# Kernel tuning notes

Hardware: AMD Instinct MI355X
Metric: run time of the kernel (lower is better)

## Reference

```python
import jax, jax.numpy as jnp
import numpy as np

N_NODES = 2176
N_IN = 64
N_HID = 2048
N_OUT = 64
NODE_DIM = 64
HEADS = 4


def _build_edge_index():
    hs, os_ = N_IN, N_IN + N_HID
    # input -> hidden block (order: for i: for h)
    s1 = np.repeat(np.arange(0, N_IN), N_HID)
    t1 = np.tile(np.arange(hs, os_), N_IN)
    # hidden -> output block (order: for h: for o)
    s2 = np.repeat(np.arange(hs, os_), N_OUT)
    t2 = np.tile(np.arange(os_, N_NODES), N_HID)
    return jnp.asarray(np.stack([np.concatenate([s1, s2]), np.concatenate([t1, t2])]), dtype=jnp.int32)


def setup_inputs() -> dict:
    key = jax.random.key(0)
    ks = jax.random.split(key, 20)
    D, H = NODE_DIM, HEADS
    edge_index = _build_edge_index()  # [2, E]
    E = edge_index.shape[1]

    def xavier(k, shape):
        fan_in, fan_out = shape[0], shape[1]
        lim = float(np.sqrt(6.0 / (fan_in + fan_out)))
        return jax.random.uniform(k, shape, jnp.float32, -lim, lim)

    return {
        "x_input": jax.random.normal(ks[0], (N_IN,), jnp.float32),
        "node_features": jax.random.normal(ks[1], (N_NODES, D), jnp.float32) * 0.1,
        "edge_weights": jax.random.normal(ks[2], (E, 1), jnp.float32) * 0.1,
        "edge_index": edge_index,
        "wq1": xavier(ks[3], (D, D * H)), "wk1": xavier(ks[4], (D, D * H)),
        "wv1": xavier(ks[5], (D, D * H)), "we1": xavier(ks[6], (1, H)),
        "wo1": xavier(ks[7], (D * H, D)), "bo1": jnp.zeros((D,), jnp.float32),
        "wq2": xavier(ks[8], (D, D * H)), "wk2": xavier(ks[9], (D, D * H)),
        "wv2": xavier(ks[10], (D, D * H)), "we2": xavier(ks[11], (1, H)),
        "wo2": xavier(ks[12], (D * H, D)), "bo2": jnp.zeros((D,), jnp.float32),
        "wproj": xavier(ks[13], (D, 1)), "bproj": jnp.zeros((1,), jnp.float32),
        "num_output_nodes": N_OUT,
    }


def _message_pass(x, edge_index, ew, wq, wk, wv, we, wo, bo):
    # x: [N, D_in]; edge_index: [2, E]; ew: [E, 1]
    src, tgt = edge_index[0], edge_index[1]
    dout = wo.shape[1]
    heads = wq.shape[1] // dout
    q = (x[tgt] @ wq).reshape(-1, heads, dout)  # [E, H, D]
    k = (x[src] @ wk).reshape(-1, heads, dout)
    v = (x[src] @ wv).reshape(-1, heads, dout)
    attn = (q * k).sum(-1) / jnp.sqrt(jnp.float32(dout)) + ew @ we  # [E, H]
    # NOTE: the per-target segment-softmax in the torch source is dead code;
    # the effective math is leaky_relu then a global softmax over edges.
    attn = jax.nn.leaky_relu(attn, negative_slope=0.2)
    attn = jax.nn.softmax(attn, axis=0)
    weighted_v = (attn[:, :, None] * v).reshape(-1, heads * dout)  # [E, H*D]
    out = jax.ops.segment_sum(weighted_v, tgt, num_segments=x.shape[0])  # [N, H*D]
    out = out @ wo + bo
    return out + x  # residual (in_channels == out_channels)


def reference(x_input, node_features, edge_weights, edge_index,
              wq1, wk1, wv1, we1, wo1, bo1,
              wq2, wk2, wv2, we2, wo2, bo2,
              wproj, bproj, num_output_nodes):
    n_in = x_input.shape[0]
    x = node_features.at[:n_in, 0].set(x_input)
    x = jax.nn.relu(_message_pass(x, edge_index, edge_weights, wq1, wk1, wv1, we1, wo1, bo1))
    x = jax.nn.relu(_message_pass(x, edge_index, edge_weights, wq2, wk2, wv2, we2, wo2, bo2))
    out_nodes = x[x.shape[0] - num_output_nodes:]
    output = jax.nn.sigmoid(out_nodes @ wproj + bproj).squeeze()
    return output, x
```

## Files before the change

kernel.cpp:

```cpp
#include <hip/hip_runtime.h>
#include <math.h>

#define E1 131072

__device__ __forceinline__ void gemm_nn_acc(const float* __restrict__ A,
                                            const float* __restrict__ B,
                                            float acc[4][4], int tr, int tc) {
  for (int k4 = 0; k4 < 16; ++k4) {
    float4 b0 = *(const float4*)&B[(k4 * 4 + 0) * 68 + tc * 4];
    float4 b1 = *(const float4*)&B[(k4 * 4 + 1) * 68 + tc * 4];
    float4 b2 = *(const float4*)&B[(k4 * 4 + 2) * 68 + tc * 4];
    float4 b3 = *(const float4*)&B[(k4 * 4 + 3) * 68 + tc * 4];
#pragma unroll
    for (int a = 0; a < 4; ++a) {
      float4 av = *(const float4*)&A[(tr + 16 * a) * 68 + k4 * 4];
      acc[a][0] += av.x * b0.x + av.y * b1.x + av.z * b2.x + av.w * b3.x;
      acc[a][1] += av.x * b0.y + av.y * b1.y + av.z * b2.y + av.w * b3.y;
      acc[a][2] += av.x * b0.z + av.y * b1.z + av.z * b2.z + av.w * b3.z;
      acc[a][3] += av.x * b0.w + av.y * b1.w + av.z * b2.w + av.w * b3.w;
    }
  }
}

__device__ __forceinline__ void gemm_nt_acc(const float* __restrict__ A,
                                            const float* __restrict__ B,
                                            float acc[4][4], int tr, int tc) {
  for (int k4 = 0; k4 < 16; ++k4) {
    float4 av[4], bv[4];
#pragma unroll
    for (int a = 0; a < 4; ++a) av[a] = *(const float4*)&A[(tr + 16 * a) * 68 + k4 * 4];
#pragma unroll
    for (int b = 0; b < 4; ++b) bv[b] = *(const float4*)&B[(tc + 16 * b) * 68 + k4 * 4];
#pragma unroll
    for (int a = 0; a < 4; ++a)
#pragma unroll
      for (int b = 0; b < 4; ++b)
        acc[a][b] += av[a].x * bv[b].x + av[a].y * bv[b].y +
                     av[a].z * bv[b].z + av[a].w * bv[b].w;
  }
}

__device__ __forceinline__ void st_tile(float* __restrict__ C, const float acc[4][4],
                                        int tr, int tc) {
#pragma unroll
  for (int a = 0; a < 4; ++a)
    *(float4*)&C[(tr + 16 * a) * 68 + tc * 4] =
        make_float4(acc[a][0], acc[a][1], acc[a][2], acc[a][3]);
}

__device__ __forceinline__ void ld_x(float* __restrict__ dst, const float* __restrict__ src,
                                     int tid, bool sub, const float* __restrict__ xinp) {
  for (int t4 = tid; t4 < 1024; t4 += 256) {
    int r = t4 >> 4, c0 = (t4 & 15) * 4;
    float4 v = *(const float4*)(src + t4 * 4);
    if (sub && c0 == 0) v.x = xinp[r];
    *(float4*)&dst[r * 68 + c0] = v;
  }
}

__device__ __forceinline__ void ld_w(float* __restrict__ dst, const float* __restrict__ w,
                                     int h, int tid) {
  for (int t4 = tid; t4 < 1024; t4 += 256) {
    int k = t4 >> 4, c0 = (t4 & 15) * 4;
    *(float4*)&dst[k * 68 + c0] = *(const float4*)(w + k * 256 + h * 64 + c0);
  }
}

__global__ __launch_bounds__(256) void k_attn1(const float* __restrict__ x,
                                               const float* __restrict__ xinp,
                                               const float* __restrict__ wq1,
                                               const float* __restrict__ wk1,
                                               const float* __restrict__ we1,
                                               const float* __restrict__ ew,
                                               const float* __restrict__ wq2,
                                               const float* __restrict__ wk2,
                                               const float* __restrict__ wv1,
                                               const float* __restrict__ wo1,
                                               const float* __restrict__ wv2,
                                               const float* __restrict__ wo2,
                                               float* __restrict__ AggH,
                                               float* __restrict__ part,
                                               float* __restrict__ bsum,
                                               float* __restrict__ Mb,
                                               float* __restrict__ W2b) {
  __shared__ float A[4352];
  __shared__ float B[4352];
  __shared__ float C[4352];
  __shared__ float D[4352];
  __shared__ float Ew[4352];
  __shared__ float F[4352];
  __shared__ float G[4352];
  __shared__ float wred[4];
  const int bid = blockIdx.x, tid = threadIdx.x;
  const bool r1 = bid < 128;
  const int tile = (r1 ? bid : bid - 128) >> 2;
  const int h = bid & 3;
  const int j0 = tile * 64;
  const int rowSrc = r1 ? 0 : (64 + j0);
  const int rowQ = r1 ? (64 + j0) : 2112;
  const int tr = tid >> 4, tc = tid & 15;
  const float weh = we1[h];

  ld_x(A, x + rowSrc * 64, tid, r1, xinp);
  ld_x(B, x + rowQ * 64, tid, false, nullptr);
  ld_w(Ew, wk1, h, tid);
  ld_w(F, wq1, h, tid);
  if (r1) {
    for (int t4 = tid; t4 < 1024; t4 += 256) {
      int i = t4 >> 4, jl0 = (t4 & 15) * 4;
      *(float4*)&G[i * 68 + jl0] = *(const float4*)(ew + i * 2048 + j0 + jl0);
    }
  } else {
    for (int t4 = tid; t4 < 1024; t4 += 256) {
      int jl = t4 >> 4, o0 = (t4 & 15) * 4;
      *(float4*)&G[jl * 68 + o0] = *(const float4*)(ew + E1 + (j0 + jl) * 64 + o0);
    }
  }
  __syncthreads();

  {
    float kt[4][4];
#pragma unroll
    for (int a = 0; a < 4; ++a)
#pragma unroll
      for (int q = 0; q < 4; ++q) kt[a][q] = 0.f;
    gemm_nn_acc(A, Ew, kt, tr, tc);
    st_tile(C, kt, tr, tc);
    float qt[4][4];
#pragma unroll
    for (int a = 0; a < 4; ++a)
#pragma unroll
      for (int q = 0; q < 4; ++q) qt[a][q] = 0.f;
    gemm_nn_acc(B, F, qt, tr, tc);
    st_tile(D, qt, tr, tc);
  }
  __syncthreads();

  float acc[4][4];
#pragma unroll
  for (int a = 0; a < 4; ++a)
#pragma unroll
    for (int b = 0; b < 4; ++b) acc[a][b] = 0.f;
  gemm_nt_acc(D, C, acc, tr, tc);
  float esum = 0.f;
#pragma unroll
  for (int a = 0; a < 4; ++a) {
    int row = tr + 16 * a;
#pragma unroll
    for (int b = 0; b < 4; ++b) {
      int col = tc + 16 * b;
      float v = acc[a][b] * 0.125f + G[col * 68 + row] * weh;
      v = (v >= 0.f) ? v : 0.2f * v;
      v = fminf(v, 60.f);
      float e = __expf(v);
      esum += e;
      B[row * 68 + col] = e;
    }
  }
#pragma unroll
  for (int s = 1; s < 64; s <<= 1) esum += __shfl_xor(esum, s);
  if ((tid & 63) == 0) wred[tid >> 6] = esum;
  __syncthreads();

  float u[4][4];
#pragma unroll
  for (int a = 0; a < 4; ++a)
#pragma unroll
    for (int q = 0; q < 4; ++q) u[a][q] = 0.f;
  gemm_nn_acc(B, A, u, tr, tc);
  if (r1) {
#pragma unroll
    for (int a = 0; a < 4; ++a)
      *(float4*)&AggH[(j0 + tr + 16 * a) * 256 + h * 64 + tc * 4] =
          make_float4(u[a][0], u[a][1], u[a][2], u[a][3]);
  } else {
#pragma unroll
    for (int a = 0; a < 4; ++a)
      *(float4*)&part[tile * 16384 + (tr + 16 * a) * 256 + h * 64 + tc * 4] =
          make_float4(u[a][0], u[a][1], u[a][2], u[a][3]);
  }
  if (tid == 0) bsum[bid] = (wred[0] + wred[1]) + (wred[2] + wred[3]);

  if (bid < 12) {
    __syncthreads();
    const int type = bid >> 2, hh = bid & 3;
    if (type == 0) {
      for (int t4 = tid; t4 < 1024; t4 += 256) {
        int r = t4 >> 4, c0 = (t4 & 15) * 4;
        *(float4*)&A[r * 68 + c0] = *(const float4*)(wq2 + r * 256 + hh * 64 + c0);
        *(float4*)&B[r * 68 + c0] = *(const float4*)(wk2 + r * 256 + hh * 64 + c0);
      }
      __syncthreads();
      float m[4][4];
#pragma unroll
      for (int a = 0; a < 4; ++a)
#pragma unroll
        for (int b = 0; b < 4; ++b) m[a][b] = 0.f;
      gemm_nt_acc(A, B, m, tr, tc);
#pragma unroll
      for (int a = 0; a < 4; ++a)
#pragma unroll
        for (int b = 0; b < 4; ++b)
          Mb[hh * 4096 + (tr + 16 * a) * 64 + tc + 16 * b] = m[a][b];
    } else {
      const float* wv = (type == 1) ? wv1 : wv2;
      const float* wo = (type == 1) ? wo1 : wo2;
      for (int t4 = tid; t4 < 1024; t4 += 256) {
        int r = t4 >> 4, c0 = (t4 & 15) * 4;
        *(float4*)&A[r * 68 + c0] = *(const float4*)(wv + r * 256 + hh * 64 + c0);
        *(float4*)&B[r * 68 + c0] = *(const float4*)(wo + (hh * 64 + r) * 64 + c0);
      }
      __syncthreads();
      float m[4][4];
#pragma unroll
      for (int a = 0; a < 4; ++a)
#pragma unroll
        for (int b = 0; b < 4; ++b) m[a][b] = 0.f;
      gemm_nn_acc(A, B, m, tr, tc);
      float* o = W2b + (type - 1) * 16384;
#pragma unroll
      for (int a = 0; a < 4; ++a)
        *(float4*)&o[(hh * 64 + tr + 16 * a) * 64 + tc * 4] =
            make_float4(m[a][0], m[a][1], m[a][2], m[a][3]);
    }
  }
}

__global__ __launch_bounds__(256) void k_attn2(const float* __restrict__ x,
                                               const float* __restrict__ Mb,
                                               const float* __restrict__ we,
                                               const float* __restrict__ ew,
                                               float* __restrict__ AggH,
                                               float* __restrict__ part,
                                               float* __restrict__ bsum) {
  __shared__ float A[4352];
  __shared__ float B[4352];
  __shared__ float C[4352];
  __shared__ float D[4352];
  __shared__ float Em[4352];
  __shared__ float wred[4];
  const int bid = blockIdx.x, tid = threadIdx.x;
  const bool r1 = bid < 128;
  const int tile = (r1 ? bid : bid - 128) >> 2;
  const int h = bid & 3;
  const int j0 = tile * 64;
  const int rowSrc = r1 ? 0 : (64 + j0);
  const int rowQ = r1 ? (64 + j0) : 2112;
  const int tr = tid >> 4, tc = tid & 15;
  const float weh = we[h];
  const float* Mh = Mb + h * 4096;

  ld_x(A, x + rowSrc * 64, tid, false, nullptr);
  ld_x(B, x + rowQ * 64, tid, false, nullptr);
  for (int t4 = tid; t4 < 1024; t4 += 256) {
    int r = t4 >> 4, c0 = (t4 & 15) * 4;
    *(float4*)&Em[r * 68 + c0] = *(const float4*)(Mh + r * 64 + c0);
  }
  if (r1) {
    for (int t4 = tid; t4 < 1024; t4 += 256) {
      int i = t4 >> 4, jl0 = (t4 & 15) * 4;
      *(float4*)&D[i * 68 + jl0] = *(const float4*)(ew + i * 2048 + j0 + jl0);
    }
  } else {
    for (int t4 = tid; t4 < 1024; t4 += 256) {
      int jl = t4 >> 4, o0 = (t4 & 15) * 4;
      *(float4*)&D[jl * 68 + o0] = *(const float4*)(ew + E1 + (j0 + jl) * 64 + o0);
    }
  }
  __syncthreads();

  {
    float t_[4][4];
#pragma unroll
    for (int a = 0; a < 4; ++a)
#pragma unroll
      for (int q = 0; q < 4; ++q) t_[a][q] = 0.f;
    gemm_nn_acc(B, Em, t_, tr, tc);
    st_tile(C, t_, tr, tc);
  }
  __syncthreads();

  float acc[4][4];
#pragma unroll
  for (int a = 0; a < 4; ++a)
#pragma unroll
    for (int b = 0; b < 4; ++b) acc[a][b] = 0.f;
  gemm_nt_acc(C, A, acc, tr, tc);
  float esum = 0.f;
#pragma unroll
  for (int a = 0; a < 4; ++a) {
    int row = tr + 16 * a;
#pragma unroll
    for (int b = 0; b < 4; ++b) {
      int col = tc + 16 * b;
      float v = acc[a][b] * 0.125f + D[col * 68 + row] * weh;
      v = (v >= 0.f) ? v : 0.2f * v;
      v = fminf(v, 60.f);
      float e = __expf(v);
      esum += e;
      B[row * 68 + col] = e;
    }
  }
#pragma unroll
  for (int s = 1; s < 64; s <<= 1) esum += __shfl_xor(esum, s);
  if ((tid & 63) == 0) wred[tid >> 6] = esum;
  __syncthreads();

  float u[4][4];
#pragma unroll
  for (int a = 0; a < 4; ++a)
#pragma unroll
    for (int q = 0; q < 4; ++q) u[a][q] = 0.f;
  gemm_nn_acc(B, A, u, tr, tc);
  if (r1) {
#pragma unroll
    for (int a = 0; a < 4; ++a)
      *(float4*)&AggH[(j0 + tr + 16 * a) * 256 + h * 64 + tc * 4] =
          make_float4(u[a][0], u[a][1], u[a][2], u[a][3]);
  } else {
#pragma unroll
    for (int a = 0; a < 4; ++a)
      *(float4*)&part[tile * 16384 + (tr + 16 * a) * 256 + h * 64 + tc * 4] =
          make_float4(u[a][0], u[a][1], u[a][2], u[a][3]);
  }
  if (tid == 0) bsum[bid] = (wred[0] + wred[1]) + (wred[2] + wred[3]);
}

template<bool SUB, bool HEAD>
__global__ __launch_bounds__(256) void k_proj(const float* __restrict__ xin,
                                              const float* __restrict__ xinp,
                                              const float* __restrict__ AggH,
                                              const float* __restrict__ part,
                                              const float* __restrict__ bsum,
                                              const float* __restrict__ W2,
                                              const float* __restrict__ bo,
                                              const float* __restrict__ wproj,
                                              const float* __restrict__ bproj,
                                              float* __restrict__ xout,
                                              float* __restrict__ outh) {
  __shared__ float As[4][260];
  const int bid = blockIdx.x, tid = threadIdx.x;
  const int n0 = bid * 4;
  const int nl = tid >> 6, d = tid & 63;
  const int node = n0 + nl;

  float inv[4];
  {
    int l = tid & 63;
#pragma unroll
    for (int hh = 0; hh < 4; ++hh) {
      float s = (l < 32) ? bsum[l * 4 + hh] : bsum[128 + (l - 32) * 4 + hh];
#pragma unroll
      for (int st = 1; st < 64; st <<= 1) s += __shfl_xor(s, st);
      inv[hh] = 1.f / s;
    }
  }

  float xres = xin[node * 64 + d];
  if (SUB) {
    if (d == 0 && node < 64) xres = xinp[node];
  }

  float val;
  if (n0 < 64) {
    val = xres + bo[d];
  } else {
    if (n0 < 2112) {
      int a = tid >> 6, c0 = (tid & 63) * 4;
      float4 v = *(const float4*)&AggH[(n0 - 64 + a) * 256 + c0];
      float iv = inv[c0 >> 6];
      *(float4*)&As[a][c0] = make_float4(v.x * iv, v.y * iv, v.z * iv, v.w * iv);
    } else {
      int a = tid >> 6, c0 = (tid & 63) * 4;
      float4 s = make_float4(0.f, 0.f, 0.f, 0.f);
      for (int ch = 0; ch < 32; ++ch) {
        float4 v = *(const float4*)&part[ch * 16384 + (n0 - 2112 + a) * 256 + c0];
        s.x += v.x; s.y += v.y; s.z += v.z; s.w += v.w;
      }
      float iv = inv[c0 >> 6];
      *(float4*)&As[a][c0] = make_float4(s.x * iv, s.y * iv, s.z * iv, s.w * iv);
    }
    __syncthreads();
    float acc = xres + bo[d];
    for (int c4 = 0; c4 < 64; ++c4) {
      float4 a4 = *(const float4*)&As[nl][c4 * 4];
      acc += a4.x * W2[(c4 * 4 + 0) * 64 + d] + a4.y * W2[(c4 * 4 + 1) * 64 + d] +
             a4.z * W2[(c4 * 4 + 2) * 64 + d] + a4.w * W2[(c4 * 4 + 3) * 64 + d];
    }
    val = acc;
  }
  val = fmaxf(val, 0.f);
  xout[node * 64 + d] = val;

  if (HEAD) {
    if (n0 >= 2112) {
      float wv = val * wproj[d];
#pragma unroll
      for (int st = 1; st < 64; st <<= 1) wv += __shfl_xor(wv, st);
      if ((tid & 63) == 0) outh[node - 2112] = 1.f / (1.f + __expf(-(wv + bproj[0])));
    }
  }
}

extern "C" void kernel_launch(void* const* d_in, const int* in_sizes, int n_in,
                              void* d_out, int out_size, void* d_ws, size_t ws_size,
                              hipStream_t stream) {
  const float* x_input       = (const float*)d_in[0];
  const float* node_features = (const float*)d_in[1];
  const float* edge_weights  = (const float*)d_in[2];
  const float* wq1 = (const float*)d_in[4];
  const float* wk1 = (const float*)d_in[5];
  const float* wv1 = (const float*)d_in[6];
  const float* we1 = (const float*)d_in[7];
  const float* wo1 = (const float*)d_in[8];
  const float* bo1 = (const float*)d_in[9];
  const float* wq2 = (const float*)d_in[10];
  const float* wk2 = (const float*)d_in[11];
  const float* wv2 = (const float*)d_in[12];
  const float* we2 = (const float*)d_in[13];
  const float* wo2 = (const float*)d_in[14];
  const float* bo2 = (const float*)d_in[15];
  const float* wproj = (const float*)d_in[16];
  const float* bproj = (const float*)d_in[17];

  float* out = (float*)d_out;
  float* ws = (float*)d_ws;
  float* xB   = ws;
  float* AggH = xB + 139264;
  float* part = AggH + 524288;
  float* bsum = part + 524288;
  float* Mb   = bsum + 256;
  float* W2b  = Mb + 16384;

  k_attn1<<<256, 256, 0, stream>>>(node_features, x_input, wq1, wk1, we1, edge_weights,
                                   wq2, wk2, wv1, wo1, wv2, wo2,
                                   AggH, part, bsum, Mb, W2b);
  k_proj<true, false><<<544, 256, 0, stream>>>(node_features, x_input, AggH, part, bsum,
                                               W2b, bo1, nullptr, nullptr, xB, nullptr);
  k_attn2<<<256, 256, 0, stream>>>(xB, Mb, we2, edge_weights, AggH, part, bsum);
  k_proj<false, true><<<544, 256, 0, stream>>>(xB, nullptr, AggH, part, bsum,
                                               W2b + 16384, bo2, wproj, bproj, out + 64, out);
}
```

Before: 58.15 us.

## Double block threads, shrink LDS, precompute layer-2 input-node key products

The attention kernels now run 512 threads per block, with each thread owning a 2x4 sub-tile instead of 4x4. LDS use drops from seven 64x68 buffers to three by reusing them across phases, with extra barriers between phases. Layer-2 logits for the input-node block are precomputed once in k_attn1 as Y1p = relu(x_in + bo1)·Wk2·Wq2^T, which is valid because input nodes have no incoming edges. k_attn2 then does one GEMM for those tiles instead of two. This aims at better occupancy and latency hiding plus less work, at the cost of more synchronisation and heavier setup blocks.

```diff
diff --git a/kernel.cpp b/kernel.cpp
--- a/kernel.cpp
+++ b/kernel.cpp
@@ -3,17 +3,18 @@
 
 #define E1 131072
 
-__device__ __forceinline__ void gemm_nn_acc(const float* __restrict__ A,
-                                            const float* __restrict__ B,
-                                            float acc[4][4], int tr, int tc) {
-  for (int k4 = 0; k4 < 16; ++k4) {
+template<int K4>
+__device__ __forceinline__ void nn2(const float* __restrict__ A,
+                                    const float* __restrict__ B,
+                                    float acc[2][4], int tr, int tc) {
+  for (int k4 = 0; k4 < K4; ++k4) {
     float4 b0 = *(const float4*)&B[(k4 * 4 + 0) * 68 + tc * 4];
     float4 b1 = *(const float4*)&B[(k4 * 4 + 1) * 68 + tc * 4];
     float4 b2 = *(const float4*)&B[(k4 * 4 + 2) * 68 + tc * 4];
     float4 b3 = *(const float4*)&B[(k4 * 4 + 3) * 68 + tc * 4];
 #pragma unroll
-    for (int a = 0; a < 4; ++a) {
-      float4 av = *(const float4*)&A[(tr + 16 * a) * 68 + k4 * 4];
+    for (int a = 0; a < 2; ++a) {
+      float4 av = *(const float4*)&A[(tr + 32 * a) * 68 + k4 * 4];
       acc[a][0] += av.x * b0.x + av.y * b1.x + av.z * b2.x + av.w * b3.x;
       acc[a][1] += av.x * b0.y + av.y * b1.y + av.z * b2.y + av.w * b3.y;
       acc[a][2] += av.x * b0.z + av.y * b1.z + av.z * b2.z + av.w * b3.z;
@@ -22,17 +23,17 @@
   }
 }
 
-__device__ __forceinline__ void gemm_nt_acc(const float* __restrict__ A,
-                                            const float* __restrict__ B,
-                                            float acc[4][4], int tr, int tc) {
+__device__ __forceinline__ void nt2(const float* __restrict__ A,
+                                    const float* __restrict__ B,
+                                    float acc[2][4], int tr, int tc) {
   for (int k4 = 0; k4 < 16; ++k4) {
-    float4 av[4], bv[4];
-#pragma unroll
-    for (int a = 0; a < 4; ++a) av[a] = *(const float4*)&A[(tr + 16 * a) * 68 + k4 * 4];
+    float4 av[2], bv[4];
+#pragma unroll
+    for (int a = 0; a < 2; ++a) av[a] = *(const float4*)&A[(tr + 32 * a) * 68 + k4 * 4];
 #pragma unroll
     for (int b = 0; b < 4; ++b) bv[b] = *(const float4*)&B[(tc + 16 * b) * 68 + k4 * 4];
 #pragma unroll
-    for (int a = 0; a < 4; ++a)
+    for (int a = 0; a < 2; ++a)
 #pragma unroll
       for (int b = 0; b < 4; ++b)
         acc[a][b] += av[a].x * bv[b].x + av[a].y * bv[b].y +
@@ -40,33 +41,34 @@
   }
 }
 
-__device__ __forceinline__ void st_tile(float* __restrict__ C, const float acc[4][4],
-                                        int tr, int tc) {
-#pragma unroll
-  for (int a = 0; a < 4; ++a)
-    *(float4*)&C[(tr + 16 * a) * 68 + tc * 4] =
+__device__ __forceinline__ void st2(float* __restrict__ C, const float acc[2][4],
+                                    int tr, int tc) {
+#pragma unroll
+  for (int a = 0; a < 2; ++a)
+    *(float4*)&C[(tr + 32 * a) * 68 + tc * 4] =
         make_float4(acc[a][0], acc[a][1], acc[a][2], acc[a][3]);
 }
 
-__device__ __forceinline__ void ld_x(float* __restrict__ dst, const float* __restrict__ src,
+template<int NT>
+__device__ __forceinline__ void ld64(float* __restrict__ dst, const float* __restrict__ src,
                                      int tid, bool sub, const float* __restrict__ xinp) {
-  for (int t4 = tid; t4 < 1024; t4 += 256) {
+  for (int t4 = tid; t4 < 1024; t4 += NT) {
     int r = t4 >> 4, c0 = (t4 & 15) * 4;
     float4 v = *(const float4*)(src + t4 * 4);
     if (sub && c0 == 0) v.x = xinp[r];
     *(float4*)&dst[r * 68 + c0] = v;
   }
 }
-
-__device__ __forceinline__ void ld_w(float* __restrict__ dst, const float* __restrict__ w,
-                                     int h, int tid) {
-  for (int t4 = tid; t4 < 1024; t4 += 256) {
+template<int NT>
+__device__ __forceinline__ void ldw(float* __restrict__ dst, const float* __restrict__ w,
+                                    int h, int tid) {
+  for (int t4 = tid; t4 < 1024; t4 += NT) {
     int k = t4 >> 4, c0 = (t4 & 15) * 4;
     *(float4*)&dst[k * 68 + c0] = *(const float4*)(w + k * 256 + h * 64 + c0);
   }
 }
 
-__global__ __launch_bounds__(256) void k_attn1(const float* __restrict__ x,
+__global__ __launch_bounds__(512) void k_attn1(const float* __restrict__ x,
                                                const float* __restrict__ xinp,
                                                const float* __restrict__ wq1,
                                                const float* __restrict__ wk1,
@@ -78,78 +80,68 @@
                                                const float* __restrict__ wo1,
                                                const float* __restrict__ wv2,
                                                const float* __restrict__ wo2,
+                                               const float* __restrict__ bo1,
                                                float* __restrict__ AggH,
                                                float* __restrict__ part,
                                                float* __restrict__ bsum,
-                                               float* __restrict__ Mb,
+                                               float* __restrict__ Y1p,
+                                               float* __restrict__ M2b,
                                                float* __restrict__ W2b) {
   __shared__ float A[4352];
   __shared__ float B[4352];
-  __shared__ float C[4352];
-  __shared__ float D[4352];
-  __shared__ float Ew[4352];
-  __shared__ float F[4352];
-  __shared__ float G[4352];
-  __shared__ float wred[4];
+  __shared__ float W[4352];
+  __shared__ float wred[8];
   const int bid = blockIdx.x, tid = threadIdx.x;
+  const int h = bid & 3;
   const bool r1 = bid < 128;
   const int tile = (r1 ? bid : bid - 128) >> 2;
-  const int h = bid & 3;
   const int j0 = tile * 64;
-  const int rowSrc = r1 ? 0 : (64 + j0);
-  const int rowQ = r1 ? (64 + j0) : 2112;
   const int tr = tid >> 4, tc = tid & 15;
   const float weh = we1[h];
 
-  ld_x(A, x + rowSrc * 64, tid, r1, xinp);
-  ld_x(B, x + rowQ * 64, tid, false, nullptr);
-  ld_w(Ew, wk1, h, tid);
-  ld_w(F, wq1, h, tid);
   if (r1) {
-    for (int t4 = tid; t4 < 1024; t4 += 256) {
+    ld64<512>(A, x, tid, true, xinp);
+    ld64<512>(B, x + (64 + j0) * 64, tid, false, nullptr);
+  } else {
+    ld64<512>(A, x + (64 + j0) * 64, tid, false, nullptr);
+    ld64<512>(B, x + 2112 * 64, tid, false, nullptr);
+  }
+  ldw<512>(W, wk1, h, tid);
+  __syncthreads();
+  float kt[2][4] = {};
+  nn2<16>(A, W, kt, tr, tc);
+  __syncthreads();
+  ldw<512>(W, wq1, h, tid);
+  __syncthreads();
+  float qt[2][4] = {};
+  nn2<16>(B, W, qt, tr, tc);
+  __syncthreads();
+  st2(W, kt, tr, tc);
+  st2(B, qt, tr, tc);
+  __syncthreads();
+  float lg[2][4] = {};
+  nt2(B, W, lg, tr, tc);
+  __syncthreads();
+  if (r1) {
+    for (int t4 = tid; t4 < 1024; t4 += 512) {
       int i = t4 >> 4, jl0 = (t4 & 15) * 4;
-      *(float4*)&G[i * 68 + jl0] = *(const float4*)(ew + i * 2048 + j0 + jl0);
+      *(float4*)&W[i * 68 + jl0] = *(const float4*)(ew + i * 2048 + j0 + jl0);
     }
   } else {
-    for (int t4 = tid; t4 < 1024; t4 += 256) {
+    for (int t4 = tid; t4 < 1024; t4 += 512) {
       int jl = t4 >> 4, o0 = (t4 & 15) * 4;
-      *(float4*)&G[jl * 68 + o0] = *(const float4*)(ew + E1 + (j0 + jl) * 64 + o0);
-    }
-  }
-  __syncthreads();
-
-  {
-    float kt[4][4];
-#pragma unroll
-    for (int a = 0; a < 4; ++a)
-#pragma unroll
-      for (int q = 0; q < 4; ++q) kt[a][q] = 0.f;
-    gemm_nn_acc(A, Ew, kt, tr, tc);
-    st_tile(C, kt, tr, tc);
-    float qt[4][4];
-#pragma unroll
-    for (int a = 0; a < 4; ++a)
-#pragma unroll
-      for (int q = 0; q < 4; ++q) qt[a][q] = 0.f;
-    gemm_nn_acc(B, F, qt, tr, tc);
-    st_tile(D, qt, tr, tc);
-  }
-  __syncthreads();
-
-  float acc[4][4];
-#pragma unroll
-  for (int a = 0; a < 4; ++a)
-#pragma unroll
-    for (int b = 0; b < 4; ++b) acc[a][b] = 0.f;
-  gemm_nt_acc(D, C, acc, tr, tc);
+      *(float4*)&W[jl * 68 + o0] = *(const float4*)(ew + E1 + (j0 + jl) * 64 + o0);
+    }
+  }
+  __syncthreads();
   float esum = 0.f;
 #pragma unroll
-  for (int a = 0; a < 4; ++a) {
-    int row = tr + 16 * a;
+  for (int a = 0; a < 2; ++a) {
+    int row = tr + 32 * a;
 #pragma unroll
     for (int b = 0; b < 4; ++b) {
       int col = tc + 16 * b;
-      float v = acc[a][b] * 0.125f + G[col * 68 + row] * weh;
+      float v = lg[a][b] * 0.125f + W[col * 68 + row] * weh;
       v = (v >= 0.f) ? v : 0.2f * v;
       v = fminf(v, 60.f);
       float e = __expf(v);
@@ -161,73 +153,88 @@
   for (int s = 1; s < 64; s <<= 1) esum += __shfl_xor(esum, s);
   if ((tid & 63) == 0) wred[tid >> 6] = esum;
   __syncthreads();
-
-  float u[4][4];
-#pragma unroll
-  for (int a = 0; a < 4; ++a)
-#pragma unroll
-    for (int q = 0; q < 4; ++q) u[a][q] = 0.f;
-  gemm_nn_acc(B, A, u, tr, tc);
+  float u[2][4] = {};
+  nn2<16>(B, A, u, tr, tc);
   if (r1) {
 #pragma unroll
-    for (int a = 0; a < 4; ++a)
-      *(float4*)&AggH[(j0 + tr + 16 * a) * 256 + h * 64 + tc * 4] =
+    for (int a = 0; a < 2; ++a)
+      *(float4*)&AggH[(j0 + tr + 32 * a) * 256 + h * 64 + tc * 4] =
           make_float4(u[a][0], u[a][1], u[a][2], u[a][3]);
   } else {
 #pragma unroll
-    for (int a = 0; a < 4; ++a)
-      *(float4*)&part[tile * 16384 + (tr + 16 * a) * 256 + h * 64 + tc * 4] =
+    for (int a = 0; a < 2; ++a)
+      *(float4*)&part[tile * 16384 + (tr + 32 * a) * 256 + h * 64 + tc * 4] =
           make_float4(u[a][0], u[a][1], u[a][2], u[a][3]);
   }
-  if (tid == 0) bsum[bid] = (wred[0] + wred[1]) + (wred[2] + wred[3]);
-
-  if (bid < 12) {
+  if (tid == 0) {
+    float s = 0.f;
+#pragma unroll
+    for (int i = 0; i < 8; ++i) s += wred[i];
+    bsum[bid] = s;
+  }
+
+  if (bid < 16) {
     __syncthreads();
     const int type = bid >> 2, hh = bid & 3;
     if (type == 0) {
-      for (int t4 = tid; t4 < 1024; t4 += 256) {
+      for (int t4 = tid; t4 < 1024; t4 += 512) {
         int r = t4 >> 4, c0 = (t4 & 15) * 4;
-        *(float4*)&A[r * 68 + c0] = *(const float4*)(wq2 + r * 256 + hh * 64 + c0);
-        *(float4*)&B[r * 68 + c0] = *(const float4*)(wk2 + r * 256 + hh * 64 + c0);
+        float4 v = *(const float4*)(x + t4 * 4);
+        if (c0 == 0) v.x = xinp[r];
+        float4 bv = *(const float4*)(bo1 + c0);
+        v.x = fmaxf(v.x + bv.x, 0.f); v.y = fmaxf(v.y + bv.y, 0.f);
+        v.z = fmaxf(v.z + bv.z, 0.f); v.w = fmaxf(v.w + bv.w, 0.f);
+        *(float4*)&A[r * 68 + c0] = v;
+      }
+      ldw<512>(W, wk2, hh, tid);
+      __syncthreads();
+      float t_[2][4] = {};
+      nn2<16>(A, W, t_, tr, tc);
+      __syncthreads();
+      st2(A, t_, tr, tc);
+      ldw<512>(W, wq2, hh, tid);
+      __syncthreads();
+      float y[2][4] = {};
+      nt2(A, W, y, tr, tc);
+#pragma unroll
+      for (int a = 0; a < 2; ++a)
+#pragma unroll
+        for (int b = 0; b < 4; ++b)
+          Y1p[hh * 4096 + (tr + 32 * a) * 64 + tc + 16 * b] = y[a][b];
+    } else if (type == 1) {
+      ldw<512>(A, wq2, hh, tid);
+      ldw<512>(W, wk2, hh, tid);
+      __syncthreads();
+      float m[2][4] = {};
+      nt2(A, W, m, tr, tc);
+#pragma unroll
+      for (int a = 0; a < 2; ++a)
+#pragma unroll
+        for (int b = 0; b < 4; ++b)
+          M2b[hh * 4096 + (tr + 32 * a) * 64 + tc + 16 * b] = m[a][b];
+    } else {
+      const float* wv = (type == 2) ? wv1 : wv2;
+      const float* wo = (type == 2) ? wo1 : wo2;
+      ldw<512>(A, wv, hh, tid);
+      for (int t4 = tid; t4 < 1024; t4 += 512) {
+        int t = t4 >> 4, c0 = (t4 & 15) * 4;
+        *(float4*)&W[t * 68 + c0] = *(const float4*)(wo + (hh * 64 + t) * 64 + c0);
       }
       __syncthreads();
-      float m[4][4];
-#pragma unroll
-      for (int a = 0; a < 4; ++a)
-#pragma unroll
-        for (int b = 0; b < 4; ++b) m[a][b] = 0.f;
-      gemm_nt_acc(A, B, m, tr, tc);
-#pragma unroll
-      for (int a = 0; a < 4; ++a)
-#pragma unroll
-        for (int b = 0; b < 4; ++b)
-          Mb[hh * 4096 + (tr + 16 * a) * 64 + tc + 16 * b] = m[a][b];
-    } else {
-      const float* wv = (type == 1) ? wv1 : wv2;
-      const float* wo = (type == 1) ? wo1 : wo2;
-      for (int t4 = tid; t4 < 1024; t4 += 256) {
-        int r = t4 >> 4, c0 = (t4 & 15) * 4;
-        *(float4*)&A[r * 68 + c0] = *(const float4*)(wv + r * 256 + hh * 64 + c0);
-        *(float4*)&B[r * 68 + c0] = *(const float4*)(wo + (hh * 64 + r) * 64 + c0);
-      }
-      __syncthreads();
-      float m[4][4];
-#pragma unroll
-      for (int a = 0; a < 4; ++a)
-#pragma unroll
-        for (int b = 0; b < 4; ++b) m[a][b] = 0.f;
-      gemm_nn_acc(A, B, m, tr, tc);
-      float* o = W2b + (type - 1) * 16384;
-#pragma unroll
-      for (int a = 0; a < 4; ++a)
-        *(float4*)&o[(hh * 64 + tr + 16 * a) * 64 + tc * 4] =
+      float m[2][4] = {};
+      nn2<16>(A, W, m, tr, tc);
+      float* o = W2b + (type - 2) * 16384;
+#pragma unroll
+      for (int a = 0; a < 2; ++a)
+        *(float4*)&o[(hh * 64 + tr + 32 * a) * 64 + tc * 4] =
             make_float4(m[a][0], m[a][1], m[a][2], m[a][3]);
     }
   }
 }
 
-__global__ __launch_bounds__(256) void k_attn2(const float* __restrict__ x,
-                                               const float* __restrict__ Mb,
+__global__ __launch_bounds__(512) void k_attn2(const float* __restrict__ x,
+                                               const float* __restrict__ Y1p,
+                                               const float* __restrict__ M2b,
                                                const float* __restrict__ we,
                                                const float* __restrict__ ew,
                                                float* __restrict__ AggH,
@@ -235,95 +242,109 @@
                                                float* __restrict__ bsum) {
   __shared__ float A[4352];
   __shared__ float B[4352];
-  __shared__ float C[4352];
-  __shared__ float D[4352];
-  __shared__ float Em[4352];
-  __shared__ float wred[4];
+  __shared__ float W[4352];
+  __shared__ float wred[8];
   const int bid = blockIdx.x, tid = threadIdx.x;
+  const int h = bid & 3;
   const bool r1 = bid < 128;
   const int tile = (r1 ? bid : bid - 128) >> 2;
-  const int h = bid & 3;
   const int j0 = tile * 64;
-  const int rowSrc = r1 ? 0 : (64 + j0);
-  const int rowQ = r1 ? (64 + j0) : 2112;
   const int tr = tid >> 4, tc = tid & 15;
   const float weh = we[h];
-  const float* Mh = Mb + h * 4096;
-
-  ld_x(A, x + rowSrc * 64, tid, false, nullptr);
-  ld_x(B, x + rowQ * 64, tid, false, nullptr);
-  for (int t4 = tid; t4 < 1024; t4 += 256) {
-    int r = t4 >> 4, c0 = (t4 & 15) * 4;
-    *(float4*)&Em[r * 68 + c0] = *(const float4*)(Mh + r * 64 + c0);
-  }
+
   if (r1) {
-    for (int t4 = tid; t4 < 1024; t4 += 256) {
+    ld64<512>(A, x, tid, false, nullptr);
+    ld64<512>(B, x + (64 + j0) * 64, tid, false, nullptr);
+    ld64<512>(W, Y1p + h * 4096, tid, false, nullptr);
+    __syncthreads();
+    float lg[2][4] = {};
+    nt2(B, W, lg, tr, tc);
+    __syncthreads();
+    for (int t4 = tid; t4 < 1024; t4 += 512) {
       int i = t4 >> 4, jl0 = (t4 & 15) * 4;
-      *(float4*)&D[i * 68 + jl0] = *(const float4*)(ew + i * 2048 + j0 + jl0);
+      *(float4*)&W[i * 68 + jl0] = *(const float4*)(ew + i * 2048 + j0 + jl0);
+    }
+    __syncthreads();
+    float esum = 0.f;
+#pragma unroll
+    for (int a = 0; a < 2; ++a) {
+      int row = tr + 32 * a;
+#pragma unroll
+      for (int b = 0; b < 4; ++b) {
+        int col = tc + 16 * b;
+        float v = lg[a][b] * 0.125f + W[col * 68 + row] * weh;
+        v = (v >= 0.f) ? v : 0.2f * v;
+        v = fminf(v, 60.f);
+        float e = __expf(v);
+        esum += e;
+        B[row * 68 + col] = e;
+      }
+    }
+#pragma unroll
+    for (int s = 1; s < 64; s <<= 1) esum += __shfl_xor(esum, s);
+    if ((tid & 63) == 0) wred[tid >> 6] = esum;
+    __syncthreads();
+    float u[2][4] = {};
+    nn2<16>(B, A, u, tr, tc);
+#pragma unroll
+    for (int a = 0; a < 2; ++a)
+      *(float4*)&AggH[(j0 + tr + 32 * a) * 256 + h * 64 + tc * 4] =
+          make_float4(u[a][0], u[a][1], u[a][2], u[a][3]);
+    if (tid == 0) {
+      float s = 0.f;
+#pragma unroll
+      for (int i = 0; i < 8; ++i) s += wred[i];
+      bsum[bid] = s;
     }
   } else {
-    for (int t4 = tid; t4 < 1024; t4 += 256) {
+    ld64<512>(A, x + (64 + j0) * 64, tid, false, nullptr);
+    ld64<512>(B, x + 2112 * 64, tid, false, nullptr);
+    ld64<512>(W, M2b + h * 4096, tid, false, nullptr);
+    __syncthreads();
+    float t_[2][4] = {};
+    nn2<16>(B, W, t_, tr, tc);
+    __syncthreads();
+    st2(B, t_, tr, tc);
+    for (int t4 = tid; t4 < 1024; t4 += 512) {
       int jl = t4 >> 4, o0 = (t4 & 15) * 4;
-      *(float4*)&D[jl * 68 + o0] = *(const float4*)(ew + E1 + (j0 + jl) * 64 + o0);
-    }
-  }
-  __syncthreads();
-
-  {
-    float t_[4][4];
-#pragma unroll
-    for (int a = 0; a < 4; ++a)
-#pragma unroll
-      for (int q = 0; q < 4; ++q) t_[a][q] = 0.f;
-    gemm_nn_acc(B, Em, t_, tr, tc);
-    st_tile(C, t_, tr, tc);
-  }
-  __syncthreads();
-
-  float acc[4][4];
-#pragma unroll
-  for (int a = 0; a < 4; ++a)
-#pragma unroll
-    for (int b = 0; b < 4; ++b) acc[a][b] = 0.f;
-  gemm_nt_acc(C, A, acc, tr, tc);
-  float esum = 0.f;
-#pragma unroll
-  for (int a = 0; a < 4; ++a) {
-    int row = tr + 16 * a;
-#pragma unroll
-    for (int b = 0; b < 4; ++b) {
-      int col = tc + 16 * b;
-      float v = acc[a][b] * 0.125f + D[col * 68 + row] * weh;
-      v = (v >= 0.f) ? v : 0.2f * v;
-      v = fminf(v, 60.f);
-      float e = __expf(v);
-      esum += e;
-      B[row * 68 + col] = e;
-    }
-  }
-#pragma unroll
-  for (int s = 1; s < 64; s <<= 1) esum += __shfl_xor(esum, s);
-  if ((tid & 63) == 0) wred[tid >> 6] = esum;
-  __syncthreads();
-
-  float u[4][4];
-#pragma unroll
-  for (int a = 0; a < 4; ++a)
-#pragma unroll
-    for (int q = 0; q < 4; ++q) u[a][q] = 0.f;
-  gemm_nn_acc(B, A, u, tr, tc);
-  if (r1) {
-#pragma unroll
-    for (int a = 0; a < 4; ++a)
-      *(float4*)&AggH[(j0 + tr + 16 * a) * 256 + h * 64 + tc * 4] =
+      *(float4*)&W[jl * 68 + o0] = *(const float4*)(ew + E1 + (j0 + jl) * 64 + o0);
+    }
+    __syncthreads();
+    float lg[2][4] = {};
+    nt2(B, A, lg, tr, tc);
+    __syncthreads();
+    float esum = 0.f;
+#pragma unroll
+    for (int a = 0; a < 2; ++a) {
+      int row = tr + 32 * a;
+#pragma unroll
+      for (int b = 0; b < 4; ++b) {
+        int col = tc + 16 * b;
+        float v = lg[a][b] * 0.125f + W[col * 68 + row] * weh;
+        v = (v >= 0.f) ? v : 0.2f * v;
+        v = fminf(v, 60.f);
+        float e = __expf(v);
+        esum += e;
+        B[row * 68 + col] = e;
+      }
+    }
+#pragma unroll
+    for (int s = 1; s < 64; s <<= 1) esum += __shfl_xor(esum, s);
+    if ((tid & 63) == 0) wred[tid >> 6] = esum;
+    __syncthreads();
+    float u[2][4] = {};
+    nn2<16>(B, A, u, tr, tc);
+#pragma unroll
+    for (int a = 0; a < 2; ++a)
+      *(float4*)&part[tile * 16384 + (tr + 32 * a) * 256 + h * 64 + tc * 4] =
           make_float4(u[a][0], u[a][1], u[a][2], u[a][3]);
-  } else {
-#pragma unroll
-    for (int a = 0; a < 4; ++a)
-      *(float4*)&part[tile * 16384 + (tr + 16 * a) * 256 + h * 64 + tc * 4] =
-          make_float4(u[a][0], u[a][1], u[a][2], u[a][3]);
-  }
-  if (tid == 0) bsum[bid] = (wred[0] + wred[1]) + (wred[2] + wred[3]);
+    if (tid == 0) {
+      float s = 0.f;
+#pragma unroll
+      for (int i = 0; i < 8; ++i) s += wred[i];
+      bsum[bid] = s;
+    }
+  }
 }
 
 template<bool SUB, bool HEAD>
@@ -365,20 +386,19 @@
   if (n0 < 64) {
     val = xres + bo[d];
   } else {
+    int a = tid >> 6, c0 = (tid & 63) * 4;
     if (n0 < 2112) {
-      int a = tid >> 6, c0 = (tid & 63) * 4;
       float4 v = *(const float4*)&AggH[(n0 - 64 + a) * 256 + c0];
       float iv = inv[c0 >> 6];
       *(float4*)&As[a][c0] = make_float4(v.x * iv, v.y * iv, v.z * iv, v.w * iv);
     } else {
-      int a = tid >> 6, c0 = (tid & 63) * 4;
-      float4 s = make_float4(0.f, 0.f, 0.f, 0.f);
+      float4 s4 = make_float4(0.f, 0.f, 0.f, 0.f);
       for (int ch = 0; ch < 32; ++ch) {
         float4 v = *(const float4*)&part[ch * 16384 + (n0 - 2112 + a) * 256 + c0];
-        s.x += v.x; s.y += v.y; s.z += v.z; s.w += v.w;
+        s4.x += v.x; s4.y += v.y; s4.z += v.z; s4.w += v.w;
       }
       float iv = inv[c0 >> 6];
-      *(float4*)&As[a][c0] = make_float4(s.x * iv, s.y * iv, s.z * iv, s.w * iv);
+      *(float4*)&As[a][c0] = make_float4(s4.x * iv, s4.y * iv, s4.z * iv, s4.w * iv);
     }
     __syncthreads();
     float acc = xres + bo[d];
@@ -429,15 +449,16 @@
   float* AggH = xB + 139264;
   float* part = AggH + 524288;
   float* bsum = part + 524288;
-  float* Mb   = bsum + 256;
-  float* W2b  = Mb + 16384;
-
-  k_attn1<<<256, 256, 0, stream>>>(node_features, x_input, wq1, wk1, we1, edge_weights,
-                                   wq2, wk2, wv1, wo1, wv2, wo2,
-                                   AggH, part, bsum, Mb, W2b);
+  float* Y1p  = bsum + 256;
+  float* M2b  = Y1p + 16384;
+  float* W2b  = M2b + 16384;
+
+  k_attn1<<<256, 512, 0, stream>>>(node_features, x_input, wq1, wk1, we1, edge_weights,
+                                   wq2, wk2, wv1, wo1, wv2, wo2, bo1,
+                                   AggH, part, bsum, Y1p, M2b, W2b);
   k_proj<true, false><<<544, 256, 0, stream>>>(node_features, x_input, AggH, part, bsum,
                                                W2b, bo1, nullptr, nullptr, xB, nullptr);
-  k_attn2<<<256, 256, 0, stream>>>(xB, Mb, we2, edge_weights, AggH, part, bsum);
+  k_attn2<<<256, 512, 0, stream>>>(xB, Y1p, M2b, we2, edge_weights, AggH, part, bsum);
   k_proj<false, true><<<544, 256, 0, stream>>>(xB, nullptr, AggH, part, bsum,
                                                W2b + 16384, bo2, wproj, bproj, out + 64, out);
 }
```

Measured after the change: 131.1 us. 125% more time.
